# Kernel optimization log

Hardware: AMD Instinct MI355X
Metric: run time of the kernel (lower is better)

Reference implementation:

```python
import jax, jax.numpy as jnp
import numpy as np

G = 512          # fine grid size
N_FINE = 150000  # target active fine voxels
THRESH = 0.8     # scn PPN Selection threshold


def _keys(c, g):
    c = c.astype(np.int64)
    return (c[:, 0] * g + c[:, 1]) * g + c[:, 2]


def _neighbors(coords, g):
    # coords: [N,3] int. Returns [N,27] neighbor indices; N == missing sentinel.
    keys = _keys(coords, g)
    order = np.argsort(keys)
    skeys = keys[order]
    N = coords.shape[0]
    offs = np.array([[dx, dy, dz] for dx in (-1, 0, 1) for dy in (-1, 0, 1) for dz in (-1, 0, 1)], np.int64)
    nbr = np.full((N, 27), N, np.int64)
    for k, o in enumerate(offs):
        nc = coords + o
        valid = np.all((nc >= 0) & (nc < g), axis=1)
        nk = _keys(np.clip(nc, 0, g - 1), g)
        pos = np.clip(np.searchsorted(skeys, nk), 0, N - 1)
        found = valid & (skeys[pos] == nk)
        nbr[:, k] = np.where(found, order[pos], N)
    return nbr


def _lookup(query, table, g):
    keys = _keys(table, g)
    order = np.argsort(keys)
    sk = keys[order]
    qk = _keys(query, g)
    pos = np.clip(np.searchsorted(sk, qk), 0, len(sk) - 1)
    return order[pos]


def setup_inputs() -> dict:
    rng = np.random.default_rng(0)
    pts = rng.integers(0, G, size=(2 * N_FINE, 3))
    fine = np.unique(pts, axis=0)[:N_FINE]              # stride-1 active sites
    mid = np.unique(fine // 4, axis=0)                  # stride-4 active sites
    coarse = np.unique(fine // 16, axis=0)              # stride-16 active sites
    N1, N2, N3 = coarse.shape[0], mid.shape[0], fine.shape[0]

    nbr1 = _neighbors(coarse, G // 16)
    nbr2 = _neighbors(mid, G // 4)
    nbr3 = _neighbors(fine, G)
    parent2 = _lookup(mid // 4, coarse, G // 16)        # middle voxel -> coarse parent
    parent3 = _lookup(fine // 4, mid, G // 4)           # fine voxel -> middle parent

    key = jax.random.key(0)
    ks = jax.random.split(key, 12)

    def w(k, shape):
        fan_in = shape[0] * shape[1]
        return jax.random.normal(k, shape, jnp.float32) / np.sqrt(fan_in)

    def coords4(c):  # prepend batch-id column (all batch 0) like get_spatial_locations
        return jnp.asarray(np.concatenate([c, np.zeros((c.shape[0], 1), c.dtype)], 1), jnp.int32)

    return {
        'feat1': jax.random.normal(ks[0], (N1, 80), jnp.float32),
        'feat2': jax.random.normal(ks[1], (N2, 48), jnp.float32),
        'feat3': jax.random.normal(ks[2], (N3, 16), jnp.float32),
        'W1': w(ks[3], (27, 80, 80)), 'W1s': w(ks[4], (27, 80, 2)),
        'W2': w(ks[5], (27, 48, 48)), 'W2s': w(ks[6], (27, 48, 2)),
        'W3': w(ks[7], (27, 16, 16)), 'W3p': w(ks[8], (27, 16, 3)),
        'W3s': w(ks[9], (27, 16, 2)), 'W3t': w(ks[10], (27, 16, 5)),
        'nbr1': jnp.asarray(nbr1, jnp.int32), 'nbr2': jnp.asarray(nbr2, jnp.int32),
        'nbr3': jnp.asarray(nbr3, jnp.int32),
        'parent2': jnp.asarray(parent2, jnp.int32), 'parent3': jnp.asarray(parent3, jnp.int32),
        'coords1': coords4(coarse), 'coords2': coords4(mid),
    }


def subconv(feat, nbr, W):
    # Submanifold 3^3 conv: out only at active sites; missing neighbors -> 0 (padded row).
    fp = jnp.concatenate([feat, jnp.zeros((1, feat.shape[1]), feat.dtype)], 0)
    g = fp[nbr]                               # [N, 27, Cin]
    return jnp.einsum('nkc,kcd->nd', g, W)    # [N, Cout]


def reference(feat1, feat2, feat3, W1, W1s, W2, W2s, W3, W3p, W3s, W3t,
              nbr1, nbr2, nbr3, parent2, parent3, coords1, coords2):
    # --- PPN1 on coarsest decoder features ---
    y = subconv(feat1, nbr1, W1)
    s1 = subconv(y, nbr1, W1s)                              # ppn1_scores [N1,2]
    mask1 = (jax.nn.softmax(s1, axis=1)[:, 1:] > THRESH).astype(feat1.dtype)  # Selection
    att1 = mask1[parent2]                                   # UnPooling x2: coarse -> middle
    # --- PPN2 on middle decoder features ---
    y2 = subconv(feat2 * att1, nbr2, W2)                    # Multiply then conv
    s2 = subconv(y2, nbr2, W2s)                             # ppn2_scores [N2,2]
    mask2 = (jax.nn.softmax(s2, axis=1)[:, 1:] > THRESH).astype(feat1.dtype)
    att2 = mask2[parent3]                                   # UnPooling x2: middle -> fine
    # --- PPN3 on finest decoder features ---
    z = subconv(feat3 * att2, nbr3, W3)
    pixel_pred = subconv(z, nbr3, W3p)                      # [N3,3]
    scores = subconv(z, nbr3, W3s)                          # [N3,2]
    ptype = subconv(z, nbr3, W3t)                           # [N3,5]
    points = jnp.concatenate([pixel_pred, scores, ptype], axis=1)
    ppn1 = jnp.concatenate([coords1.astype(jnp.float32), s1], axis=1)
    ppn2 = jnp.concatenate([coords2.astype(jnp.float32), s2], axis=1)
    return points, ppn1, ppn2, mask1, mask2
```

## Files before the change

kernel.cpp:

```cpp
#include <hip/hip_runtime.h>

typedef _Float16 f16;
typedef _Float16 f16x8 __attribute__((ext_vector_type(8)));
typedef float f32x4 __attribute__((ext_vector_type(4)));

#define LN4 1.3862943611198906f

__device__ __forceinline__ void gl_lds16(const void* g, void* l) {
    typedef unsigned int u32;
    __builtin_amdgcn_global_load_lds(
        (const __attribute__((address_space(1))) u32*)(g),
        (__attribute__((address_space(3))) u32*)(l), 16, 0, 0);
}

template<int CIN>
__global__ __launch_bounds__(256) void prep_wt(
    const float* __restrict__ W, f16* __restrict__ dst)
{
    const int RE = 2 * CIN;
    int total = CIN * 28 * CIN;
    for (int i = blockIdx.x * 256 + threadIdx.x; i < total; i += gridDim.x * 256) {
        int d = i / (28 * CIN);
        int rem = i - d * (28 * CIN);
        int tap = rem / CIN;
        int c = rem - tap * CIN;
        float v = (tap < 27) ? W[(size_t)(tap * CIN + c) * CIN + d] : 0.f;
        f16 h = (f16)v;
        size_t base = (size_t)d * (28 * RE) + (size_t)tap * RE;
        dst[base + c] = h;
        dst[base + CIN + c] = (f16)(v - (float)h);
    }
}

template<int CIN, int COUT>
__global__ __launch_bounds__(256) void prep_frag(
    const float* __restrict__ Wa, int ca, f16* __restrict__ FT)
{
    constexpr int KB = (2 * CIN) / 32;
    int total = 14 * KB * 1024;
    for (int i = blockIdx.x * 256 + threadIdx.x; i < total; i += gridDim.x * 256) {
        int j = i & 7;
        int lane = (i >> 3) & 63;
        int term = (i >> 9) & 1;
        int kbp = i >> 10;
        int kb = kbp % KB, p = kbp / KB;
        int k = kb * 32 + ((lane >> 4) * 8) + j;
        int ts = (k >= CIN) ? 1 : 0;
        int kk = k - ts * CIN;
        int tap = 2 * p + ts;
        int col = lane & 15;
        float v = 0.f;
        if (tap < 27 && col < COUT && col < ca) {
            int kc = tap * CIN + kk;
            v = Wa[(size_t)kc * ca + col];
        }
        f16 h = (f16)v;
        FT[i] = term ? (f16)(v - (float)h) : h;
    }
}

template<int CIN>
__global__ __launch_bounds__(256) void split_gated(
    const float* __restrict__ f, const float* __restrict__ mask,
    const int* __restrict__ parent, f16* __restrict__ Fc, int N)
{
    int i = blockIdx.x * 256 + threadIdx.x;
    if (i >= (N + 1) * CIN) return;
    int n = i / CIN, c = i - n * CIN;
    float v = 0.f;
    if (n < N) {
        bool a = parent ? (mask[parent[n]] != 0.f) : true;
        v = a ? f[i] : 0.f;
    }
    f16 h = (f16)v;
    Fc[(size_t)n * (2 * CIN) + c] = h;
    Fc[(size_t)n * (2 * CIN) + CIN + c] = (f16)(v - (float)h);
}

__global__ __launch_bounds__(256) void ppn_finalize_kernel(
    const int* __restrict__ coords, const float* __restrict__ s,
    float* __restrict__ ppn, float* __restrict__ mask, int N)
{
    int n = blockIdx.x * 256 + threadIdx.x;
    if (n >= N) return;
    float s0 = s[(size_t)n * 2 + 0], s1 = s[(size_t)n * 2 + 1];
    ppn[(size_t)n * 6 + 0] = (float)coords[(size_t)n * 4 + 0];
    ppn[(size_t)n * 6 + 1] = (float)coords[(size_t)n * 4 + 1];
    ppn[(size_t)n * 6 + 2] = (float)coords[(size_t)n * 4 + 2];
    ppn[(size_t)n * 6 + 3] = (float)coords[(size_t)n * 4 + 3];
    ppn[(size_t)n * 6 + 4] = s0;
    ppn[(size_t)n * 6 + 5] = s1;
    mask[n] = (s1 - s0 > LN4) ? 1.0f : 0.0f;
}

__global__ __launch_bounds__(256) void gate_kernel(
    const float* __restrict__ mask, const int* __restrict__ parent,
    float* __restrict__ act, int N)
{
    int i = blockIdx.x * 256 + threadIdx.x;
    if (i < N) act[i] = mask[parent[i]];
}

template<bool FSRC>
__global__ __launch_bounds__(256) void expand_kernel(
    const void* __restrict__ src, const int* __restrict__ nbr,
    int* __restrict__ flag, int N)
{
    int m = blockIdx.x * 256 + threadIdx.x;
    if (m >= N) return;
    bool a = FSRC ? (((const float*)src)[m] != 0.f) : (((const int*)src)[m] != 0);
    if (!a) return;
    #pragma unroll 1
    for (int t = 0; t < 27; ++t) {
        int idx = nbr[(size_t)m * 27 + t];
        if (idx < N) flag[idx] = 1;
    }
}

__global__ __launch_bounds__(256) void compact_kernel(
    const int* __restrict__ flag, int* __restrict__ list,
    int* __restrict__ cnt, int N)
{
    int i = blockIdx.x * 256 + threadIdx.x;
    int lane = threadIdx.x & 63;
    bool f = (i < N) && (flag[i] != 0);
    unsigned long long m = __ballot(f);
    int base = 0;
    if (lane == 0 && m) base = atomicAdd(cnt, __popcll(m));
    base = __shfl(base, 0);
    if (f) list[base + __popcll(m & ((1ull << lane) - 1ull))] = i;
}

template<int CIN>
__global__ __launch_bounds__(256, 3) void conv_tile(
    const f16* __restrict__ F, const int* __restrict__ nbr,
    const f16* __restrict__ WT, f16* __restrict__ Y, int N, int nTiles)
{
    constexpr int RE = 2 * CIN;
    constexpr int KB = RE / 32;
    constexpr int CT = CIN / 16;
    constexpr int CPT = RE / 8;
    constexpr int CPR = 2 * CPT;
    constexpr int PB = CPR * 16;
    __shared__ __align__(16) char BS[CIN * PB];

    const int t = threadIdx.x;
    const int lane = t & 63;
    const int l16 = lane & 15;
    const int quad = lane >> 4;
    const int wv = t >> 6;

    int q8 = (nTiles + 7) >> 3;
    int tile = (blockIdx.x & 7) * q8 + (blockIdx.x >> 3);
    if (tile >= nTiles) return;
    const int m0 = tile * 64;
    const int grow = m0 + wv * 16 + l16;

    f16x8 ahA[KB], alA[KB], ahB[KB], alB[KB];

    auto loadA = [&](int p, f16x8 (&ah)[KB], f16x8 (&al)[KB]) {
        int i0 = N, i1 = N;
        if (grow < N) {
            i0 = nbr[(size_t)grow * 27 + 2 * p];
            if (2 * p + 1 < 27) i1 = nbr[(size_t)grow * 27 + 2 * p + 1];
        }
        #pragma unroll
        for (int kb = 0; kb < KB; ++kb) {
            int ko = kb * 32 + quad * 8;
            int ts = ko >= CIN;
            int c2 = ko - (ts ? CIN : 0);
            const f16* ap = F + (size_t)(ts ? i1 : i0) * RE + c2;
            ah[kb] = *(const f16x8*)ap;
            al[kb] = *(const f16x8*)(ap + CIN);
        }
    };

    auto stageB = [&](int p) {
        for (int i = t; i < CIN * CPR; i += 256) {
            int d = i / CPR, cs = i - d * CPR;
            int c = (cs & ~7) | ((cs ^ d) & 7);
            int tp = c / CPT, cc = c - tp * CPT;
            gl_lds16((const char*)WT + (((size_t)d * 28 + 2 * p + tp) * RE + cc * 8) * 2,
                     BS + (size_t)i * 16);
        }
    };

    f32x4 acc[CT];
    #pragma unroll
    for (int ct = 0; ct < CT; ++ct) acc[ct] = (f32x4){0.f, 0.f, 0.f, 0.f};

    auto compute = [&](f16x8 (&ah)[KB], f16x8 (&al)[KB]) {
        #pragma unroll
        for (int kb = 0; kb < KB; ++kb) {
            int ko = kb * 32 + quad * 8;
            int ts = ko >= CIN;
            int c2 = ko - (ts ? CIN : 0);
            int ch = ts * CPT + c2 / 8;
            int chl = ch + CIN / 8;
            #pragma unroll
            for (int ct = 0; ct < CT; ++ct) {
                int drow = ct * 16 + l16;
                int sb = (ch & ~7) | ((ch ^ drow) & 7);
                int sbl = (chl & ~7) | ((chl ^ drow) & 7);
                f16x8 bh = *(const f16x8*)(BS + drow * PB + sb * 16);
                f16x8 bl = *(const f16x8*)(BS + drow * PB + sbl * 16);
                acc[ct] = __builtin_amdgcn_mfma_f32_16x16x32_f16(ah[kb], bh, acc[ct], 0, 0, 0);
                acc[ct] = __builtin_amdgcn_mfma_f32_16x16x32_f16(al[kb], bh, acc[ct], 0, 0, 0);
                acc[ct] = __builtin_amdgcn_mfma_f32_16x16x32_f16(ah[kb], bl, acc[ct], 0, 0, 0);
            }
        }
    };

    loadA(0, ahA, alA);
    #pragma unroll 1
    for (int p = 0; p < 14; p += 2) {
        __syncthreads();
        stageB(p);
        loadA(p + 1, ahB, alB);
        __syncthreads();
        compute(ahA, alA);

        __syncthreads();
        stageB(p + 1);
        if (p + 2 < 14) loadA(p + 2, ahA, alA);
        __syncthreads();
        compute(ahB, alB);
    }

    #pragma unroll
    for (int ct = 0; ct < CT; ++ct) {
        #pragma unroll
        for (int r = 0; r < 4; ++r) {
            int row = m0 + wv * 16 + quad * 4 + r;
            if (row < N) {
                int d = ct * 16 + l16;
                float v = acc[ct][r];
                f16 h = (f16)v;
                Y[(size_t)row * RE + d] = h;
                Y[(size_t)row * RE + CIN + d] = (f16)(v - (float)h);
            }
        }
    }
}

template<int CIN, int COUT>
__global__ __launch_bounds__(256) void score_tile(
    const f16* __restrict__ Y, const int* __restrict__ nbr,
    const f16* __restrict__ FT, float* __restrict__ S, int N, int nTiles)
{
    constexpr int RE = 2 * CIN;
    constexpr int KB = RE / 32;

    const int t = threadIdx.x;
    const int lane = t & 63;
    const int l16 = lane & 15;
    const int quad = lane >> 4;
    const int wv = t >> 6;

    int q8 = (nTiles + 7) >> 3;
    int tile = (blockIdx.x & 7) * q8 + (blockIdx.x >> 3);
    if (tile >= nTiles) return;
    const int m0 = tile * 64;
    const int grow = m0 + wv * 16 + l16;
    const bool gv = grow < N;

    f32x4 acc = (f32x4){0.f, 0.f, 0.f, 0.f};

    #pragma unroll 1
    for (int p = 0; p < 14; ++p) {
        int i0 = N, i1 = N;
        if (gv) {
            i0 = nbr[(size_t)grow * 27 + 2 * p];
            if (2 * p + 1 < 27) i1 = nbr[(size_t)grow * 27 + 2 * p + 1];
        }
        #pragma unroll
        for (int kb = 0; kb < KB; ++kb) {
            int ko = kb * 32 + quad * 8;
            int ts = ko >= CIN;
            int c2 = ko - (ts ? CIN : 0);
            const f16* ap = Y + (size_t)(ts ? i1 : i0) * RE + c2;
            f16x8 ah = *(const f16x8*)ap;
            f16x8 al = *(const f16x8*)(ap + CIN);
            const f16* fb = FT + (size_t)(p * KB + kb) * 1024 + lane * 8;
            f16x8 bh = *(const f16x8*)fb;
            f16x8 bl = *(const f16x8*)(fb + 512);
            acc = __builtin_amdgcn_mfma_f32_16x16x32_f16(ah, bh, acc, 0, 0, 0);
            acc = __builtin_amdgcn_mfma_f32_16x16x32_f16(al, bh, acc, 0, 0, 0);
            acc = __builtin_amdgcn_mfma_f32_16x16x32_f16(ah, bl, acc, 0, 0, 0);
        }
    }

    if (l16 < COUT) {
        #pragma unroll
        for (int r = 0; r < 4; ++r) {
            int row = m0 + wv * 16 + quad * 4 + r;
            if (row < N) S[(size_t)row * COUT + l16] = acc[r];
        }
    }
}

__global__ __launch_bounds__(256) void lvl3_z_compute(
    const float* __restrict__ feat3, const int* __restrict__ nbr3,
    const float* __restrict__ act, const float* __restrict__ W3,
    float* __restrict__ z, const int* __restrict__ list,
    const int* __restrict__ cnt, int N)
{
    const int lane = threadIdx.x & 63;
    const int wid0 = (blockIdx.x * 256 + threadIdx.x) >> 6;
    const int nw = (gridDim.x * 256) >> 6;
    const int count = *cnt;
    const int c = lane;

    for (int w = wid0; w < count; w += nw) {
        const int n = list[w];
        int ld = N;
        if (lane < 27) ld = nbr3[(size_t)n * 27 + lane];
        bool valid = (lane < 27) && (ld < N);
        float a = valid ? act[ld] : 0.f;
        unsigned long long m = __ballot(a != 0.f);

        float acc = 0.f;
        while (m) {
            int t = __ffsll(m) - 1; m &= m - 1;
            int idx = __shfl(ld, t);
            const float4* f4 = (const float4*)(feat3 + (size_t)idx * 16);
            const float* wgt = W3 + (size_t)t * 256;
            #pragma unroll
            for (int q = 0; q < 4; ++q) {
                float4 fv = f4[q];
                if (c < 16) {
                    acc += fv.x * wgt[(4 * q + 0) * 16 + c];
                    acc += fv.y * wgt[(4 * q + 1) * 16 + c];
                    acc += fv.z * wgt[(4 * q + 2) * 16 + c];
                    acc += fv.w * wgt[(4 * q + 3) * 16 + c];
                }
            }
        }
        if (lane < 16) z[(size_t)n * 16 + lane] = acc;
    }
}

__global__ __launch_bounds__(256) void lvl3_pts_compute(
    const float* __restrict__ z, const int* __restrict__ zflag,
    const int* __restrict__ nbr3,
    const float* __restrict__ Wp, const float* __restrict__ Ws,
    const float* __restrict__ Wt, float* __restrict__ points,
    const int* __restrict__ list, const int* __restrict__ cnt, int N)
{
    const int lane = threadIdx.x & 63;
    const int wid0 = (blockIdx.x * 256 + threadIdx.x) >> 6;
    const int nw = (gridDim.x * 256) >> 6;
    const int count = *cnt;
    const int c = lane;

    for (int w = wid0; w < count; w += nw) {
        const int n = list[w];
        int ld = N;
        if (lane < 27) ld = nbr3[(size_t)n * 27 + lane];
        bool valid = (lane < 27) && (ld < N);
        int zf = valid ? zflag[ld] : 0;
        unsigned long long m = __ballot(zf != 0);

        float acc = 0.f;
        while (m) {
            int t = __ffsll(m) - 1; m &= m - 1;
            int idx = __shfl(ld, t);
            const float4* z4 = (const float4*)(z + (size_t)idx * 16);
            #pragma unroll
            for (int q = 0; q < 4; ++q) {
                float4 zv = z4[q];
                if (c < 10) {
                    #pragma unroll
                    for (int j = 0; j < 4; ++j) {
                        int k = 4 * q + j;
                        int kc = t * 16 + k;
                        float wv = (c < 3) ? Wp[(size_t)kc * 3 + c]
                                 : (c < 5) ? Ws[(size_t)kc * 2 + (c - 3)]
                                           : Wt[(size_t)kc * 5 + (c - 5)];
                        float zj = (j == 0) ? zv.x : (j == 1) ? zv.y : (j == 2) ? zv.z : zv.w;
                        acc += zj * wv;
                    }
                }
            }
        }
        if (lane < 10) points[(size_t)n * 10 + lane] = acc;
    }
}

extern "C" void kernel_launch(void* const* d_in, const int* in_sizes, int n_in,
                              void* d_out, int out_size, void* d_ws, size_t ws_size,
                              hipStream_t stream)
{
    const float* feat1 = (const float*)d_in[0];
    const float* feat2 = (const float*)d_in[1];
    const float* feat3 = (const float*)d_in[2];
    const float* W1    = (const float*)d_in[3];
    const float* W1s   = (const float*)d_in[4];
    const float* W2    = (const float*)d_in[5];
    const float* W2s   = (const float*)d_in[6];
    const float* W3    = (const float*)d_in[7];
    const float* W3p   = (const float*)d_in[8];
    const float* W3s   = (const float*)d_in[9];
    const float* W3t   = (const float*)d_in[10];
    const int* nbr1    = (const int*)d_in[11];
    const int* nbr2    = (const int*)d_in[12];
    const int* nbr3    = (const int*)d_in[13];
    const int* parent2 = (const int*)d_in[14];
    const int* parent3 = (const int*)d_in[15];
    const int* coords1 = (const int*)d_in[16];
    const int* coords2 = (const int*)d_in[17];

    const int N1 = in_sizes[0] / 80;
    const int N2 = in_sizes[1] / 48;
    const int N3 = in_sizes[2] / 16;

    float* out = (float*)d_out;
    float* o_points = out;
    float* o_ppn1   = o_points + (size_t)N3 * 10;
    float* o_ppn2   = o_ppn1 + (size_t)N1 * 6;
    float* o_mask1  = o_ppn2 + (size_t)N2 * 6;
    float* o_mask2  = o_mask1 + (size_t)N1;

    char* wp = (char*)d_ws;
    auto alloc = [&](size_t bytes) -> char* {
        char* r = wp; wp += (bytes + 255) & ~(size_t)255; return r;
    };
    auto A256 = [](size_t b) { return (b + 255) & ~(size_t)255; };

    f16*   WT1 = (f16*)alloc((size_t)80 * 28 * 160 * 2);
    f16*   WT2 = (f16*)alloc((size_t)48 * 28 * 96 * 2);
    f16*   FT1 = (f16*)alloc((size_t)14 * 5 * 1024 * 2);
    f16*   FT2 = (f16*)alloc((size_t)14 * 3 * 1024 * 2);
    float* s1  = (float*)alloc((size_t)N1 * 2 * 4);
    float* s2  = (float*)alloc((size_t)N2 * 2 * 4);
    float* act3 = (float*)alloc((size_t)N3 * 4);
    int*   cnts = (int*)alloc(2 * 4);

    size_t e1 = (size_t)(N1 + 1) * 160, e2 = (size_t)(N2 + 1) * 96;
    size_t eF = e1 > e2 ? e1 : e2;
    f16* Fa = (f16*)alloc(eF * 2);

    size_t l3b = 4 * A256((size_t)N3 * 4) + A256((size_t)N3 * 16 * 4);
    size_t eY = eF * 2 > l3b ? eF * 2 : l3b;
    char* Yu = alloc(eY);
    f16* Y = (f16*)Yu;
    char* q3 = Yu;
    int*   flagz = (int*)q3; q3 += A256((size_t)N3 * 4);
    int*   listz = (int*)q3; q3 += A256((size_t)N3 * 4);
    int*   flagp = (int*)q3; q3 += A256((size_t)N3 * 4);
    int*   listp = (int*)q3; q3 += A256((size_t)N3 * 4);
    float* zbuf  = (float*)q3;

    auto cdiv = [](long long a, long long b) { return (int)((a + b - 1) / b); };

    hipMemsetAsync(Y + (size_t)N1 * 160, 0, 160 * 2, stream);
    hipMemsetAsync(Y + (size_t)N2 * 96, 0, 96 * 2, stream);
    hipMemsetAsync(cnts, 0, 2 * 4, stream);
    hipMemsetAsync(o_points, 0, (size_t)N3 * 10 * 4, stream);

    prep_wt<80><<<700, 256, 0, stream>>>(W1, WT1);
    prep_wt<48><<<cdiv(48 * 28 * 48, 256), 256, 0, stream>>>(W2, WT2);
    prep_frag<80, 2><<<cdiv(14 * 5 * 1024, 256), 256, 0, stream>>>(W1s, 2, FT1);
    prep_frag<48, 2><<<cdiv(14 * 3 * 1024, 256), 256, 0, stream>>>(W2s, 2, FT2);

    {
        int T = cdiv(N1, 64);
        dim3 grid(8 * cdiv(T, 8));
        split_gated<80><<<cdiv((size_t)(N1 + 1) * 80, 256), 256, 0, stream>>>(
            feat1, nullptr, nullptr, Fa, N1);
        conv_tile<80><<<grid, 256, 0, stream>>>(Fa, nbr1, WT1, Y, N1, T);
        score_tile<80, 2><<<grid, 256, 0, stream>>>(Y, nbr1, FT1, s1, N1, T);
    }
    ppn_finalize_kernel<<<cdiv(N1, 256), 256, 0, stream>>>(coords1, s1, o_ppn1, o_mask1, N1);

    {
        int T = cdiv(N2, 64);
        dim3 grid(8 * cdiv(T, 8));
        split_gated<48><<<cdiv((size_t)(N2 + 1) * 48, 256), 256, 0, stream>>>(
            feat2, o_mask1, parent2, Fa, N2);
        conv_tile<48><<<grid, 256, 0, stream>>>(Fa, nbr2, WT2, Y, N2, T);
        score_tile<48, 2><<<grid, 256, 0, stream>>>(Y, nbr2, FT2, s2, N2, T);
    }
    ppn_finalize_kernel<<<cdiv(N2, 256), 256, 0, stream>>>(coords2, s2, o_ppn2, o_mask2, N2);

    hipMemsetAsync(flagz, 0, (size_t)N3 * 4, stream);
    hipMemsetAsync(flagp, 0, (size_t)N3 * 4, stream);
    hipMemsetAsync(zbuf, 0, (size_t)N3 * 16 * 4, stream);
    gate_kernel<<<cdiv(N3, 256), 256, 0, stream>>>(o_mask2, parent3, act3, N3);
    expand_kernel<true><<<cdiv(N3, 256), 256, 0, stream>>>(act3, nbr3, flagz, N3);
    compact_kernel<<<cdiv(N3, 256), 256, 0, stream>>>(flagz, listz, &cnts[0], N3);
    lvl3_z_compute<<<2048, 256, 0, stream>>>(feat3, nbr3, act3, W3, zbuf,
                                             listz, &cnts[0], N3);
    expand_kernel<false><<<cdiv(N3, 256), 256, 0, stream>>>(flagz, nbr3, flagp, N3);
    compact_kernel<<<cdiv(N3, 256), 256, 0, stream>>>(flagp, listp, &cnts[1], N3);
    lvl3_pts_compute<<<2048, 256, 0, stream>>>(zbuf, flagz, nbr3, W3p, W3s, W3t,
                                               o_points, listp, &cnts[1], N3);
}
```

Measured before the change: 403.9 us.

## Reformulate score conv as dense per-tap GEMM plus gather-sum; two row-tiles per level-2 conv block

The 2-channel score subconv no longer gathers 27 neighbor rows for a tiny-N MFMA. Instead, each voxel's features are multiplied once by all 27 taps' weights at once (54 outputs) through a dense GEMM, and a finalize kernel sums the matching tap columns from the neighbors' rows. This removes redundant gathers of wide feature rows in exchange for writing and reading an N×54 fp32 intermediate. The level-2 conv also processes 128 rows per block so each staged weight tile is reused across twice as many rows, at the cost of more registers. The padded-row memsets are dropped, which relies on the sentinel row being handled differently now.

```diff
diff --git a/kernel.cpp b/kernel.cpp
--- a/kernel.cpp
+++ b/kernel.cpp
@@ -32,30 +32,30 @@
     }
 }
 
-template<int CIN, int COUT>
-__global__ __launch_bounds__(256) void prep_frag(
-    const float* __restrict__ Wa, int ca, f16* __restrict__ FT)
+template<int CIN>
+__global__ __launch_bounds__(256) void prep_gfrag(
+    const float* __restrict__ Ws, f16* __restrict__ FG)
 {
     constexpr int KB = (2 * CIN) / 32;
-    int total = 14 * KB * 1024;
+    int total = 2 * KB * 4 * 512;
     for (int i = blockIdx.x * 256 + threadIdx.x; i < total; i += gridDim.x * 256) {
         int j = i & 7;
         int lane = (i >> 3) & 63;
-        int term = (i >> 9) & 1;
-        int kbp = i >> 10;
-        int kb = kbp % KB, p = kbp / KB;
-        int k = kb * 32 + ((lane >> 4) * 8) + j;
-        int ts = (k >= CIN) ? 1 : 0;
-        int kk = k - ts * CIN;
-        int tap = 2 * p + ts;
-        int col = lane & 15;
-        float v = 0.f;
-        if (tap < 27 && col < COUT && col < ca) {
-            int kc = tap * CIN + kk;
-            v = Wa[(size_t)kc * ca + col];
-        }
-        f16 h = (f16)v;
-        FT[i] = term ? (f16)(v - (float)h) : h;
+        int blk = i >> 9;
+        int ct = blk & 3;
+        int kbp = blk >> 2;
+        int kb = kbp % KB;
+        int pass = kbp / KB;
+        int k = kb * 32 + ((lane >> 4) << 3) + j;
+        int col = ct * 16 + (lane & 15);
+        int c = (k < CIN) ? k : k - CIN;
+        float w = 0.f;
+        if (col < 54) {
+            int t = col >> 1, jj = col & 1;
+            w = Ws[((size_t)t * CIN + c) * 2 + jj];
+        }
+        f16 wh = (f16)w;
+        FG[i] = (pass == 0) ? wh : ((k < CIN) ? (f16)(w - (float)wh) : (f16)0.f);
     }
 }
 
@@ -75,22 +75,6 @@
     f16 h = (f16)v;
     Fc[(size_t)n * (2 * CIN) + c] = h;
     Fc[(size_t)n * (2 * CIN) + CIN + c] = (f16)(v - (float)h);
-}
-
-__global__ __launch_bounds__(256) void ppn_finalize_kernel(
-    const int* __restrict__ coords, const float* __restrict__ s,
-    float* __restrict__ ppn, float* __restrict__ mask, int N)
-{
-    int n = blockIdx.x * 256 + threadIdx.x;
-    if (n >= N) return;
-    float s0 = s[(size_t)n * 2 + 0], s1 = s[(size_t)n * 2 + 1];
-    ppn[(size_t)n * 6 + 0] = (float)coords[(size_t)n * 4 + 0];
-    ppn[(size_t)n * 6 + 1] = (float)coords[(size_t)n * 4 + 1];
-    ppn[(size_t)n * 6 + 2] = (float)coords[(size_t)n * 4 + 2];
-    ppn[(size_t)n * 6 + 3] = (float)coords[(size_t)n * 4 + 3];
-    ppn[(size_t)n * 6 + 4] = s0;
-    ppn[(size_t)n * 6 + 5] = s1;
-    mask[n] = (s1 - s0 > LN4) ? 1.0f : 0.0f;
 }
 
 __global__ __launch_bounds__(256) void gate_kernel(
@@ -131,8 +115,8 @@
     if (f) list[base + __popcll(m & ((1ull << lane) - 1ull))] = i;
 }
 
-template<int CIN>
-__global__ __launch_bounds__(256, 3) void conv_tile(
+template<int CIN, int RS>
+__global__ __launch_bounds__(256, RS == 1 ? 3 : 3) void conv_tile(
     const f16* __restrict__ F, const int* __restrict__ nbr,
     const f16* __restrict__ WT, f16* __restrict__ Y, int N, int nTiles)
 {
@@ -142,6 +126,7 @@
     constexpr int CPT = RE / 8;
     constexpr int CPR = 2 * CPT;
     constexpr int PB = CPR * 16;
+    constexpr int BM = 64 * RS;
     __shared__ __align__(16) char BS[CIN * PB];
 
     const int t = threadIdx.x;
@@ -153,25 +138,29 @@
     int q8 = (nTiles + 7) >> 3;
     int tile = (blockIdx.x & 7) * q8 + (blockIdx.x >> 3);
     if (tile >= nTiles) return;
-    const int m0 = tile * 64;
+    const int m0 = tile * BM;
     const int grow = m0 + wv * 16 + l16;
 
-    f16x8 ahA[KB], alA[KB], ahB[KB], alB[KB];
-
-    auto loadA = [&](int p, f16x8 (&ah)[KB], f16x8 (&al)[KB]) {
-        int i0 = N, i1 = N;
-        if (grow < N) {
-            i0 = nbr[(size_t)grow * 27 + 2 * p];
-            if (2 * p + 1 < 27) i1 = nbr[(size_t)grow * 27 + 2 * p + 1];
-        }
+    f16x8 ahA[RS][KB], alA[RS][KB], ahB[RS][KB], alB[RS][KB];
+
+    auto loadA = [&](int p, f16x8 (&ah)[RS][KB], f16x8 (&al)[RS][KB]) {
         #pragma unroll
-        for (int kb = 0; kb < KB; ++kb) {
-            int ko = kb * 32 + quad * 8;
-            int ts = ko >= CIN;
-            int c2 = ko - (ts ? CIN : 0);
-            const f16* ap = F + (size_t)(ts ? i1 : i0) * RE + c2;
-            ah[kb] = *(const f16x8*)ap;
-            al[kb] = *(const f16x8*)(ap + CIN);
+        for (int rs = 0; rs < RS; ++rs) {
+            int g = grow + rs * 64;
+            int i0 = N, i1 = N;
+            if (g < N) {
+                i0 = nbr[(size_t)g * 27 + 2 * p];
+                if (2 * p + 1 < 27) i1 = nbr[(size_t)g * 27 + 2 * p + 1];
+            }
+            #pragma unroll
+            for (int kb = 0; kb < KB; ++kb) {
+                int ko = kb * 32 + quad * 8;
+                int ts = ko >= CIN;
+                int c2 = ko - (ts ? CIN : 0);
+                const f16* ap = F + (size_t)(ts ? i1 : i0) * RE + c2;
+                ah[rs][kb] = *(const f16x8*)ap;
+                al[rs][kb] = *(const f16x8*)(ap + CIN);
+            }
         }
     };
 
@@ -185,11 +174,13 @@
         }
     };
 
-    f32x4 acc[CT];
+    f32x4 acc[RS][CT];
     #pragma unroll
-    for (int ct = 0; ct < CT; ++ct) acc[ct] = (f32x4){0.f, 0.f, 0.f, 0.f};
-
-    auto compute = [&](f16x8 (&ah)[KB], f16x8 (&al)[KB]) {
+    for (int rs = 0; rs < RS; ++rs)
+        #pragma unroll
+        for (int ct = 0; ct < CT; ++ct) acc[rs][ct] = (f32x4){0.f, 0.f, 0.f, 0.f};
+
+    auto compute = [&](f16x8 (&ah)[RS][KB], f16x8 (&al)[RS][KB]) {
         #pragma unroll
         for (int kb = 0; kb < KB; ++kb) {
             int ko = kb * 32 + quad * 8;
@@ -204,9 +195,12 @@
                 int sbl = (chl & ~7) | ((chl ^ drow) & 7);
                 f16x8 bh = *(const f16x8*)(BS + drow * PB + sb * 16);
                 f16x8 bl = *(const f16x8*)(BS + drow * PB + sbl * 16);
-                acc[ct] = __builtin_amdgcn_mfma_f32_16x16x32_f16(ah[kb], bh, acc[ct], 0, 0, 0);
-                acc[ct] = __builtin_amdgcn_mfma_f32_16x16x32_f16(al[kb], bh, acc[ct], 0, 0, 0);
-                acc[ct] = __builtin_amdgcn_mfma_f32_16x16x32_f16(ah[kb], bl, acc[ct], 0, 0, 0);
+                #pragma unroll
+                for (int rs = 0; rs < RS; ++rs) {
+                    acc[rs][ct] = __builtin_amdgcn_mfma_f32_16x16x32_f16(ah[rs][kb], bh, acc[rs][ct], 0, 0, 0);
+                    acc[rs][ct] = __builtin_amdgcn_mfma_f32_16x16x32_f16(al[rs][kb], bh, acc[rs][ct], 0, 0, 0);
+                    acc[rs][ct] = __builtin_amdgcn_mfma_f32_16x16x32_f16(ah[rs][kb], bl, acc[rs][ct], 0, 0, 0);
+                }
             }
         }
     };
@@ -228,25 +222,28 @@
     }
 
     #pragma unroll
-    for (int ct = 0; ct < CT; ++ct) {
+    for (int rs = 0; rs < RS; ++rs) {
         #pragma unroll
-        for (int r = 0; r < 4; ++r) {
-            int row = m0 + wv * 16 + quad * 4 + r;
-            if (row < N) {
-                int d = ct * 16 + l16;
-                float v = acc[ct][r];
-                f16 h = (f16)v;
-                Y[(size_t)row * RE + d] = h;
-                Y[(size_t)row * RE + CIN + d] = (f16)(v - (float)h);
-            }
-        }
-    }
-}
-
-template<int CIN, int COUT>
-__global__ __launch_bounds__(256) void score_tile(
-    const f16* __restrict__ Y, const int* __restrict__ nbr,
-    const f16* __restrict__ FT, float* __restrict__ S, int N, int nTiles)
+        for (int ct = 0; ct < CT; ++ct) {
+            #pragma unroll
+            for (int r = 0; r < 4; ++r) {
+                int row = m0 + rs * 64 + wv * 16 + quad * 4 + r;
+                if (row < N) {
+                    int d = ct * 16 + l16;
+                    float v = acc[rs][ct][r];
+                    f16 h = (f16)v;
+                    Y[(size_t)row * RE + d] = h;
+                    Y[(size_t)row * RE + CIN + d] = (f16)(v - (float)h);
+                }
+            }
+        }
+    }
+}
+
+template<int CIN>
+__global__ __launch_bounds__(256) void gemm_P(
+    const f16* __restrict__ Y, const f16* __restrict__ FG,
+    float* __restrict__ P, int N, int nTiles)
 {
     constexpr int RE = 2 * CIN;
     constexpr int KB = RE / 32;
@@ -262,41 +259,64 @@
     if (tile >= nTiles) return;
     const int m0 = tile * 64;
     const int grow = m0 + wv * 16 + l16;
-    const bool gv = grow < N;
-
-    f32x4 acc = (f32x4){0.f, 0.f, 0.f, 0.f};
-
-    #pragma unroll 1
-    for (int p = 0; p < 14; ++p) {
-        int i0 = N, i1 = N;
-        if (gv) {
-            i0 = nbr[(size_t)grow * 27 + 2 * p];
-            if (2 * p + 1 < 27) i1 = nbr[(size_t)grow * 27 + 2 * p + 1];
-        }
+    const int arow = (grow < N) ? grow : N;
+    const f16* ar = Y + (size_t)arow * RE;
+
+    f32x4 acc[4];
+    #pragma unroll
+    for (int ct = 0; ct < 4; ++ct) acc[ct] = (f32x4){0.f, 0.f, 0.f, 0.f};
+
+    #pragma unroll
+    for (int kb = 0; kb < KB; ++kb) {
+        f16x8 a = *(const f16x8*)(ar + kb * 32 + quad * 8);
         #pragma unroll
-        for (int kb = 0; kb < KB; ++kb) {
-            int ko = kb * 32 + quad * 8;
-            int ts = ko >= CIN;
-            int c2 = ko - (ts ? CIN : 0);
-            const f16* ap = Y + (size_t)(ts ? i1 : i0) * RE + c2;
-            f16x8 ah = *(const f16x8*)ap;
-            f16x8 al = *(const f16x8*)(ap + CIN);
-            const f16* fb = FT + (size_t)(p * KB + kb) * 1024 + lane * 8;
-            f16x8 bh = *(const f16x8*)fb;
-            f16x8 bl = *(const f16x8*)(fb + 512);
-            acc = __builtin_amdgcn_mfma_f32_16x16x32_f16(ah, bh, acc, 0, 0, 0);
-            acc = __builtin_amdgcn_mfma_f32_16x16x32_f16(al, bh, acc, 0, 0, 0);
-            acc = __builtin_amdgcn_mfma_f32_16x16x32_f16(ah, bl, acc, 0, 0, 0);
-        }
-    }
-
-    if (l16 < COUT) {
+        for (int ct = 0; ct < 4; ++ct) {
+            f16x8 b = *(const f16x8*)(FG + ((size_t)((0 * KB + kb) * 4 + ct)) * 512 + lane * 8);
+            acc[ct] = __builtin_amdgcn_mfma_f32_16x16x32_f16(a, b, acc[ct], 0, 0, 0);
+        }
         #pragma unroll
-        for (int r = 0; r < 4; ++r) {
-            int row = m0 + wv * 16 + quad * 4 + r;
-            if (row < N) S[(size_t)row * COUT + l16] = acc[r];
-        }
-    }
+        for (int ct = 0; ct < 4; ++ct) {
+            f16x8 b = *(const f16x8*)(FG + ((size_t)((1 * KB + kb) * 4 + ct)) * 512 + lane * 8);
+            acc[ct] = __builtin_amdgcn_mfma_f32_16x16x32_f16(a, b, acc[ct], 0, 0, 0);
+        }
+    }
+
+    #pragma unroll
+    for (int ct = 0; ct < 4; ++ct) {
+        int col = ct * 16 + l16;
+        if (col < 54) {
+            #pragma unroll
+            for (int r = 0; r < 4; ++r) {
+                int row = m0 + wv * 16 + quad * 4 + r;
+                if (row < N) P[(size_t)row * 54 + col] = acc[ct][r];
+            }
+        }
+    }
+}
+
+__global__ __launch_bounds__(256) void finalize_gather(
+    const int* __restrict__ coords, const float* __restrict__ P,
+    const int* __restrict__ nbr, float* __restrict__ ppn,
+    float* __restrict__ mask, int N)
+{
+    int n = blockIdx.x * 256 + threadIdx.x;
+    if (n >= N) return;
+    float s0 = 0.f, s1 = 0.f;
+    #pragma unroll
+    for (int t = 0; t < 27; ++t) {
+        int idx = nbr[(size_t)n * 27 + t];
+        if (idx < N) {
+            float2 v = *(const float2*)(P + (size_t)idx * 54 + 2 * t);
+            s0 += v.x; s1 += v.y;
+        }
+    }
+    ppn[(size_t)n * 6 + 0] = (float)coords[(size_t)n * 4 + 0];
+    ppn[(size_t)n * 6 + 1] = (float)coords[(size_t)n * 4 + 1];
+    ppn[(size_t)n * 6 + 2] = (float)coords[(size_t)n * 4 + 2];
+    ppn[(size_t)n * 6 + 3] = (float)coords[(size_t)n * 4 + 3];
+    ppn[(size_t)n * 6 + 4] = s0;
+    ppn[(size_t)n * 6 + 5] = s1;
+    mask[n] = (s1 - s0 > LN4) ? 1.0f : 0.0f;
 }
 
 __global__ __launch_bounds__(256) void lvl3_z_compute(
@@ -429,20 +449,21 @@
 
     f16*   WT1 = (f16*)alloc((size_t)80 * 28 * 160 * 2);
     f16*   WT2 = (f16*)alloc((size_t)48 * 28 * 96 * 2);
-    f16*   FT1 = (f16*)alloc((size_t)14 * 5 * 1024 * 2);
-    f16*   FT2 = (f16*)alloc((size_t)14 * 3 * 1024 * 2);
-    float* s1  = (float*)alloc((size_t)N1 * 2 * 4);
-    float* s2  = (float*)alloc((size_t)N2 * 2 * 4);
+    f16*   FG1 = (f16*)alloc((size_t)2 * 5 * 4 * 512 * 2);
+    f16*   FG2 = (f16*)alloc((size_t)2 * 3 * 4 * 512 * 2);
     float* act3 = (float*)alloc((size_t)N3 * 4);
     int*   cnts = (int*)alloc(2 * 4);
 
-    size_t e1 = (size_t)(N1 + 1) * 160, e2 = (size_t)(N2 + 1) * 96;
-    size_t eF = e1 > e2 ? e1 : e2;
-    f16* Fa = (f16*)alloc(eF * 2);
+    size_t fa1 = (size_t)(N1 + 1) * 320, fa2 = (size_t)(N2 + 1) * 192;
+    size_t pmax = (size_t)(N1 > N2 ? N1 : N2) * 216 + 256;
+    size_t szFaP = fa1 > fa2 ? fa1 : fa2; if (pmax > szFaP) szFaP = pmax;
+    char* FaP = alloc(szFaP);
+    f16*   Fa = (f16*)FaP;
+    float* P  = (float*)FaP;
 
     size_t l3b = 4 * A256((size_t)N3 * 4) + A256((size_t)N3 * 16 * 4);
-    size_t eY = eF * 2 > l3b ? eF * 2 : l3b;
-    char* Yu = alloc(eY);
+    size_t szY = fa1 > fa2 ? fa1 : fa2; if (l3b > szY) szY = l3b;
+    char* Yu = alloc(szY);
     f16* Y = (f16*)Yu;
     char* q3 = Yu;
     int*   flagz = (int*)q3; q3 += A256((size_t)N3 * 4);
@@ -453,35 +474,37 @@
 
     auto cdiv = [](long long a, long long b) { return (int)((a + b - 1) / b); };
 
-    hipMemsetAsync(Y + (size_t)N1 * 160, 0, 160 * 2, stream);
-    hipMemsetAsync(Y + (size_t)N2 * 96, 0, 96 * 2, stream);
     hipMemsetAsync(cnts, 0, 2 * 4, stream);
     hipMemsetAsync(o_points, 0, (size_t)N3 * 10 * 4, stream);
 
     prep_wt<80><<<700, 256, 0, stream>>>(W1, WT1);
     prep_wt<48><<<cdiv(48 * 28 * 48, 256), 256, 0, stream>>>(W2, WT2);
-    prep_frag<80, 2><<<cdiv(14 * 5 * 1024, 256), 256, 0, stream>>>(W1s, 2, FT1);
-    prep_frag<48, 2><<<cdiv(14 * 3 * 1024, 256), 256, 0, stream>>>(W2s, 2, FT2);
+    prep_gfrag<80><<<80, 256, 0, stream>>>(W1s, FG1);
+    prep_gfrag<48><<<48, 256, 0, stream>>>(W2s, FG2);
 
     {
-        int T = cdiv(N1, 64);
-        dim3 grid(8 * cdiv(T, 8));
+        int Tc = cdiv(N1, 64);
+        dim3 gc(8 * cdiv(Tc, 8));
         split_gated<80><<<cdiv((size_t)(N1 + 1) * 80, 256), 256, 0, stream>>>(
             feat1, nullptr, nullptr, Fa, N1);
-        conv_tile<80><<<grid, 256, 0, stream>>>(Fa, nbr1, WT1, Y, N1, T);
-        score_tile<80, 2><<<grid, 256, 0, stream>>>(Y, nbr1, FT1, s1, N1, T);
-    }
-    ppn_finalize_kernel<<<cdiv(N1, 256), 256, 0, stream>>>(coords1, s1, o_ppn1, o_mask1, N1);
+        conv_tile<80, 1><<<gc, 256, 0, stream>>>(Fa, nbr1, WT1, Y, N1, Tc);
+        gemm_P<80><<<gc, 256, 0, stream>>>(Y, FG1, P, N1, Tc);
+        finalize_gather<<<cdiv(N1, 256), 256, 0, stream>>>(
+            coords1, P, nbr1, o_ppn1, o_mask1, N1);
+    }
 
     {
-        int T = cdiv(N2, 64);
-        dim3 grid(8 * cdiv(T, 8));
+        int Tc = cdiv(N2, 128);
+        dim3 gc(8 * cdiv(Tc, 8));
+        int Tg = cdiv(N2, 64);
+        dim3 gg(8 * cdiv(Tg, 8));
         split_gated<48><<<cdiv((size_t)(N2 + 1) * 48, 256), 256, 0, stream>>>(
             feat2, o_mask1, parent2, Fa, N2);
-        conv_tile<48><<<grid, 256, 0, stream>>>(Fa, nbr2, WT2, Y, N2, T);
-        score_tile<48, 2><<<grid, 256, 0, stream>>>(Y, nbr2, FT2, s2, N2, T);
-    }
-    ppn_finalize_kernel<<<cdiv(N2, 256), 256, 0, stream>>>(coords2, s2, o_ppn2, o_mask2, N2);
+        conv_tile<48, 2><<<gc, 256, 0, stream>>>(Fa, nbr2, WT2, Y, N2, Tc);
+        gemm_P<48><<<gg, 256, 0, stream>>>(Y, FG2, P, N2, Tg);
+        finalize_gather<<<cdiv(N2, 256), 256, 0, stream>>>(
+            coords2, P, nbr2, o_ppn2, o_mask2, N2);
+    }
 
     hipMemsetAsync(flagz, 0, (size_t)N3 * 4, stream);
     hipMemsetAsync(flagp, 0, (size_t)N3 * 4, stream);
```

After: 371.7 us. 8.0% less time.
